# Kernel tuning notes

Measured on AMD Instinct MI355X. Metric: run time of the kernel, lower is better.

## Reference

```python
import jax, jax.numpy as jnp
import numpy as np

E, S, V_OBS, OBJ, H, L, V_COMM = 64, 64, 128, 16, 256, 32, 32
K = 2 * OBJ  # expected number of nonzero indices per step


def prelu(x, a):
    return jnp.where(x >= 0, x, a * x)


def setup_inputs() -> dict:
    key = jax.random.key(0)
    ks = jax.random.split(key, 32)
    # obs: multi-hot with exactly K ones per (episode, step)
    u = jax.random.uniform(ks[0], (E, S, V_OBS))
    idx = jnp.argsort(u, axis=-1)[..., :K]
    obs = jax.nn.one_hot(idx, V_OBS, dtype=jnp.float32).sum(-2)
    comm = jax.random.normal(ks[1], (E, S, L, V_COMM), jnp.float32)

    def w(k, shape):
        return (jax.random.normal(k, shape, jnp.float32) * 0.05)

    a = lambda: jnp.asarray(0.25, jnp.float32)  # PReLU init
    b = lambda n: jnp.full((n,), 0.01, jnp.float32)
    return dict(
        obs=obs, comm=comm,
        obs_emb=w(ks[2], (V_OBS, H)), obs_a_emb=a(),
        obs_W=w(ks[3], (K * H, H)), obs_b=b(H), obs_a=a(),
        comm_emb=w(ks[4], (V_COMM, H)), comm_a_emb=a(),
        cw1=w(ks[5], (H // 4, H, 1)), cb1=b(H // 4),
        cw3=w(ks[6], (H // 4, H, 3)), cb3=b(H // 4),
        cw5=w(ks[7], (H // 4, H, 5)), cb5=b(H // 4),
        cw7=w(ks[8], (H // 4, H, 7)), cb7=b(H // 4),
        bn_g=jnp.ones((H,), jnp.float32), bn_b=jnp.zeros((H,), jnp.float32), cnn_a=a(),
        Wx=w(ks[9], (3, H, H)), bx=jnp.full((3, H), 0.01, jnp.float32),
        Wh=w(ks[10], (3, H, H)), bh=jnp.full((3, H), 0.01, jnp.float32),
        lin_a1=a(), lin_W=w(ks[11], (H, H)), lin_b=b(H), lin_a2=a(),
    )


def reference(obs, comm, obs_emb, obs_a_emb, obs_W, obs_b, obs_a,
              comm_emb, comm_a_emb, cw1, cb1, cw3, cb3, cw5, cb5, cw7, cb7,
              bn_g, bn_b, cnn_a, Wx, bx, Wh, bh, lin_a1, lin_W, lin_b, lin_a2):
    Ep, St, _ = obs.shape
    # extract_and_concatenate: ascending indices of the K ones per (episode, step)
    idx = jnp.argsort(-obs, axis=-1)[..., :K]          # stable sort -> ascending nonzero idx
    oe = prelu(obs_emb[idx], obs_a_emb)                # [E,S,K,H]
    o = prelu(oe.reshape(Ep, St, K * H) @ obs_W + obs_b, obs_a)  # [E,S,H]

    # comm path (comm already at max_comm_len, pad_zeros is identity)
    tok = jnp.argmax(comm, axis=-1)                    # [E,S,L]
    ce = prelu(comm_emb[tok], comm_a_emb)              # [E,S,L,H]
    x = ce.reshape(Ep * St, L, H).transpose(0, 2, 1)   # [N,H,L]
    dn = ('NCH', 'OIH', 'NCH')
    conv = lambda w_, b_: jax.lax.conv_general_dilated(
        x, w_, (1,), 'SAME', dimension_numbers=dn) + b_[None, :, None]
    y = jnp.concatenate([conv(cw1, cb1), conv(cw3, cb3),
                         conv(cw5, cb5), conv(cw7, cb7)], axis=1)  # [N,H,L]
    # BatchNorm1d (training-mode batch statistics over N and L)
    m = y.mean(axis=(0, 2), keepdims=True)
    v = y.var(axis=(0, 2), keepdims=True)
    y = bn_g[None, :, None] * (y - m) / jnp.sqrt(v + 1e-5) + bn_b[None, :, None]
    y = prelu(y, cnn_a).transpose(0, 2, 1)             # [N,L,H]

    # MTRNN (time_constant=True -> new=1, old=0): GRU-like gated cell
    xproj = jnp.einsum('nlh,ghk->glnk', y, Wx) + bx[:, None, None, :]  # [3,L,N,H]
    h0 = jnp.zeros((Ep * St, H), y.dtype)

    def step(h, xs):
        xr, xz, xn = xs
        r = jax.nn.sigmoid(xr + h @ Wh[0] + bh[0])
        z = jax.nn.sigmoid(xz + h @ Wh[1] + bh[1])
        n = jnp.tanh(xn + r * (h @ Wh[2] + bh[2]))
        return n * (1 - z) + h * z, None

    hN, _ = jax.lax.scan(step, h0, (xproj[0], xproj[1], xproj[2]))  # last step == outputs[:,-1]
    c = hN.reshape(Ep, St, H)
    c = prelu(prelu(c, lin_a1) @ lin_W + lin_b, lin_a2)
    return jnp.concatenate([o, c], axis=-1)           # [E,S,2H]
```

## Files before the change

kernel.cpp:

```cpp
#include <hip/hip_runtime.h>
#include <hip/hip_bf16.h>

#define N_ 4096
#define VOBS 128
#define KOBS 32
#define H_ 256
#define L_ 32
#define VCOMM 32

typedef __attribute__((ext_vector_type(8))) short short8;
typedef __attribute__((ext_vector_type(4))) float floatx4;

__device__ __forceinline__ float prelu_f(float x, float a){ return x >= 0.f ? x : a*x; }
__device__ __forceinline__ ushort f2bf(float x){
  unsigned int u = __float_as_uint(x);
  u = (u + 0x7FFFu + ((u >> 16) & 1u)) >> 16;
  return (ushort)u;
}
__device__ __forceinline__ float bf2f(ushort x){
  unsigned int u = ((unsigned int)x) << 16;
  return __uint_as_float(u);
}

__device__ __forceinline__ void gl_lds16(const ushort* __restrict__ src, ushort* dst){
  __builtin_amdgcn_global_load_lds(
      (const __attribute__((address_space(1))) unsigned int*)src,
      (__attribute__((address_space(3))) unsigned int*)dst, 16, 0, 0);
}


__global__ __launch_bounds__(256) void k_idx(const float* __restrict__ obs, int* __restrict__ idx){
  const int n = blockIdx.x*4 + (threadIdx.x >> 6);
  const int lane = threadIdx.x & 63;
  float v0 = obs[(size_t)n*VOBS + lane];
  float v1 = obs[(size_t)n*VOBS + 64 + lane];
  unsigned long long m0 = __ballot(v0 > 0.5f);
  unsigned long long m1 = __ballot(v1 > 0.5f);
  unsigned long long lt = (1ull << lane) - 1ull;
  if (v0 > 0.5f){
    int pos = __popcll(m0 & lt);
    if (pos < KOBS) idx[n*KOBS + pos] = lane;
  }
  if (v1 > 0.5f){
    int pos = __popcll(m0) + __popcll(m1 & lt);
    if (pos < KOBS) idx[n*KOBS + pos] = 64 + lane;
  }
}

__global__ __launch_bounds__(256) void k_contrib(
    const float* __restrict__ obs_emb, const float* __restrict__ a_emb_p,
    const float* __restrict__ obs_W, float* __restrict__ contrib){
  const int k = blockIdx.x;
  const int vbase = blockIdx.y*16;
  const int tid = threadIdx.x;
  __shared__ float pe[16][H_];
  float a = a_emb_p[0];
  for (int i = tid; i < 16*H_; i += 256){
    int v = i >> 8, j = i & 255;
    pe[v][j] = prelu_f(obs_emb[(size_t)(vbase+v)*H_ + j], a);
  }
  __syncthreads();
  float acc[16];
  #pragma unroll
  for (int v = 0; v < 16; ++v) acc[v] = 0.f;
  for (int j = 0; j < H_; ++j){
    float w = obs_W[((size_t)(k*H_ + j))*H_ + tid];
    #pragma unroll
    for (int v = 0; v < 16; ++v) acc[v] += pe[v][j]*w;
  }
  for (int v = 0; v < 16; ++v)
    contrib[((size_t)((vbase+v)*KOBS + k))*H_ + tid] = acc[v];
}

__global__ __launch_bounds__(256) void k_obs_o(
    const int* __restrict__ idx, const float* __restrict__ contrib,
    const float* __restrict__ obs_b, const float* __restrict__ obs_a_p,
    float* __restrict__ out){
  const int n = blockIdx.x, tid = threadIdx.x;
  __shared__ int id[KOBS];
  if (tid < KOBS) id[tid] = idx[n*KOBS + tid];
  __syncthreads();
  float acc = obs_b[tid];
  #pragma unroll 8
  for (int k = 0; k < KOBS; ++k)
    acc += contrib[((size_t)(id[k]*KOBS + k))*H_ + tid];
  out[(size_t)n*512 + tid] = prelu_f(acc, obs_a_p[0]);
}


__global__ void k_tok(const float* __restrict__ comm, int* __restrict__ tok){
  int i = blockIdx.x*blockDim.x + threadIdx.x;
  if (i >= N_*L_) return;
  const float4* p = (const float4*)(comm + (size_t)i*VCOMM);
  float best = -1e30f; int bi = 0;
  #pragma unroll
  for (int j = 0; j < 8; ++j){
    float4 q = p[j];
    if (q.x > best){ best = q.x; bi = j*4+0; }
    if (q.y > best){ best = q.y; bi = j*4+1; }
    if (q.z > best){ best = q.z; bi = j*4+2; }
    if (q.w > best){ best = q.w; bi = j*4+3; }
  }
  tok[i] = bi;
}

__global__ void k_P(const float* __restrict__ comm_emb, const float* __restrict__ ca_p,
                    const float* __restrict__ cw1, const float* __restrict__ cw3,
                    const float* __restrict__ cw5, const float* __restrict__ cw7,
                    float* __restrict__ P){
  const int slot = blockIdx.x, v = blockIdx.y, c = threadIdx.x;
  int g, tap;
  if (slot == 0){ g=0; tap=0; }
  else if (slot < 4){ g=1; tap=slot-1; }
  else if (slot < 9){ g=2; tap=slot-4; }
  else { g=3; tap=slot-9; }
  const float* w; int ks;
  if (g==0){ w=cw1; ks=1; } else if (g==1){ w=cw3; ks=3; }
  else if (g==2){ w=cw5; ks=5; } else { w=cw7; ks=7; }
  float a = ca_p[0];
  float acc = 0.f;
  for (int h = 0; h < H_; ++h){
    float e = prelu_f(comm_emb[(size_t)v*H_ + h], a);
    acc += e * w[(size_t)(c*H_ + h)*ks + tap];
  }
  P[(size_t)(slot*VCOMM + v)*64 + c] = acc;
}

template<int KS, bool APPLY>
__device__ __forceinline__ void conv_work(
    const float* __restrict__ Ps, const int tk[16][L_], int wave, int lane,
    float bias, float scale, float shift, float ca,
    ushort* __restrict__ ynorm, int nbase, int g,
    float* s_out, float* q_out)
{
  constexpr int PAD = (KS-1)/2;
  float s = 0.f, sq = 0.f;
  for (int j = 0; j < 4; ++j){
    const int nn = wave*4 + j;
    int base[L_];
    #pragma unroll
    for (int l = 0; l < L_; ++l) base[l] = tk[nn][l]*64 + lane;
    #pragma unroll
    for (int l = 0; l < L_; ++l){
      float acc = bias;
      #pragma unroll
      for (int t = 0; t < KS; ++t){
        const int lp = l + t - PAD;
        if (lp >= 0 && lp < L_) acc += Ps[t*2048 + base[lp]];
      }
      if (APPLY){
        float y = prelu_f(fmaf(acc, scale, shift), ca);
        ynorm[((size_t)l*N_ + (nbase+nn))*H_ + g*64 + lane] = f2bf(y);
      } else {
        s += acc; sq += acc*acc;
      }
    }
  }
  *s_out = s; *q_out = sq;
}

__global__ __launch_bounds__(256) void k_conv_stats(
    const int* __restrict__ tok, const float* __restrict__ P,
    const float* __restrict__ cb1, const float* __restrict__ cb3,
    const float* __restrict__ cb5, const float* __restrict__ cb7,
    float* __restrict__ stats){
  const int g = blockIdx.y;
  const int nbase = blockIdx.x*16;
  const int tid = threadIdx.x, lane = tid & 63, wave = tid >> 6;
  const int ks = 2*g + 1, base = g*g;
  const float* cb = (g==0)?cb1:(g==1)?cb3:(g==2)?cb5:cb7;
  const float bias = cb[lane];
  __shared__ float Ps[7*2048];
  __shared__ int tk[16][L_];
  __shared__ float red_s[4][64], red_q[4][64];
  for (int i = tid; i < ks*512; i += 256)
    ((float4*)Ps)[i] = ((const float4*)(P + base*2048))[i];
  for (int i = tid; i < 16*L_; i += 256)
    tk[i>>5][i&31] = tok[(size_t)(nbase + (i>>5))*L_ + (i&31)];
  __syncthreads();
  float s = 0.f, sq = 0.f;
  switch (g){
    case 0: conv_work<1,false>(Ps, tk, wave, lane, bias, 0,0,0, nullptr, nbase, g, &s, &sq); break;
    case 1: conv_work<3,false>(Ps, tk, wave, lane, bias, 0,0,0, nullptr, nbase, g, &s, &sq); break;
    case 2: conv_work<5,false>(Ps, tk, wave, lane, bias, 0,0,0, nullptr, nbase, g, &s, &sq); break;
    default: conv_work<7,false>(Ps, tk, wave, lane, bias, 0,0,0, nullptr, nbase, g, &s, &sq); break;
  }
  red_s[wave][lane] = s; red_q[wave][lane] = sq;
  __syncthreads();
  if (wave == 0){
    float ts = red_s[0][lane]+red_s[1][lane]+red_s[2][lane]+red_s[3][lane];
    float tq = red_q[0][lane]+red_q[1][lane]+red_q[2][lane]+red_q[3][lane];
    atomicAdd(&stats[g*64 + lane], ts);
    atomicAdd(&stats[256 + g*64 + lane], tq);
  }
}

__global__ void k_bn_fin(const float* __restrict__ stats, const float* __restrict__ bn_g,
                         const float* __restrict__ bn_b, float* __restrict__ ss){
  int t = threadIdx.x;
  const float cnt = (float)(N_*L_);
  float m = stats[t]/cnt;
  float v = stats[256+t]/cnt - m*m;
  float sc = bn_g[t] / sqrtf(v + 1e-5f);
  ss[t] = sc; ss[256+t] = bn_b[t] - m*sc;
}

__global__ __launch_bounds__(256) void k_conv_apply(
    const int* __restrict__ tok, const float* __restrict__ P,
    const float* __restrict__ cb1, const float* __restrict__ cb3,
    const float* __restrict__ cb5, const float* __restrict__ cb7,
    const float* __restrict__ ss, const float* __restrict__ cnn_a_p,
    ushort* __restrict__ ynorm){
  const int g = blockIdx.y;
  const int nbase = blockIdx.x*16;
  const int tid = threadIdx.x, lane = tid & 63, wave = tid >> 6;
  const int ks = 2*g + 1, base = g*g;
  const float* cb = (g==0)?cb1:(g==1)?cb3:(g==2)?cb5:cb7;
  const float bias = cb[lane];
  const float scale = ss[g*64 + lane], shift = ss[256 + g*64 + lane];
  const float ca = cnn_a_p[0];
  __shared__ float Ps[7*2048];
  __shared__ int tk[16][L_];
  for (int i = tid; i < ks*512; i += 256)
    ((float4*)Ps)[i] = ((const float4*)(P + base*2048))[i];
  for (int i = tid; i < 16*L_; i += 256)
    tk[i>>5][i&31] = tok[(size_t)(nbase + (i>>5))*L_ + (i&31)];
  __syncthreads();
  float s, q;
  switch (g){
    case 0: conv_work<1,true>(Ps, tk, wave, lane, bias, scale, shift, ca, ynorm, nbase, g, &s, &q); break;
    case 1: conv_work<3,true>(Ps, tk, wave, lane, bias, scale, shift, ca, ynorm, nbase, g, &s, &q); break;
    case 2: conv_work<5,true>(Ps, tk, wave, lane, bias, scale, shift, ca, ynorm, nbase, g, &s, &q); break;
    default: conv_work<7,true>(Ps, tk, wave, lane, bias, scale, shift, ca, ynorm, nbase, g, &s, &q); break;
  }
}


__global__ void k_WT3(const float* __restrict__ Wx, const float* __restrict__ Wh,
                      ushort* __restrict__ WxT3, ushort* __restrict__ WhT3p){
  int id = blockIdx.x*256 + threadIdx.x;
  int g = id >> 16, u = (id >> 8) & 255, k = id & 255;
  WxT3[id]  = f2bf(Wx[(size_t)g*65536 + k*256 + u]);
  WhT3p[id] = f2bf(Wh[(size_t)g*65536 + k*256 + u]);
}

__global__ __launch_bounds__(256,2) void k_xproj(
    const ushort* __restrict__ Y, const ushort* __restrict__ WxT3,
    ushort* __restrict__ xp)
{
  extern __shared__ __align__(16) char smem[];
  ushort* Bs = (ushort*)smem;
  ushort* Tb = (ushort*)smem + 33792;
  const int bm = blockIdx.x;
  const int tid = threadIdx.x, lane = tid & 63, w = tid >> 6;
  const int wm = w >> 1, wn = w & 1;
  const int quad = lane >> 4, l16 = lane & 15;

  short8 Af[4][8];
  #pragma unroll
  for (int mi = 0; mi < 4; ++mi)
    #pragma unroll
    for (int kt = 0; kt < 8; ++kt)
      Af[mi][kt] = *(const short8*)(Y + ((size_t)(bm*128 + wm*64 + mi*16 + l16))*H_ + kt*32 + quad*8);

  for (int bn = 0; bn < 6; ++bn){
    __syncthreads();
    #pragma unroll
    for (int i = 0; i < 16; ++i){
      int id = i*256 + tid;
      int row = id >> 5, cc = id & 31;
      *(uint4*)&Bs[row*264 + cc*8] = *(const uint4*)(WxT3 + ((size_t)(bn*128 + row))*H_ + cc*8);
    }
    __syncthreads();
    floatx4 acc[4][4];
    #pragma unroll
    for (int i = 0; i < 4; ++i)
      #pragma unroll
      for (int j = 0; j < 4; ++j)
        acc[i][j] = (floatx4){0.f,0.f,0.f,0.f};
    #pragma unroll
    for (int kt = 0; kt < 8; ++kt){
      short8 b[4];
      #pragma unroll
      for (int ni = 0; ni < 4; ++ni)
        b[ni] = *(const short8*)&Bs[(wn*64 + ni*16 + l16)*264 + kt*32 + quad*8];
      #pragma unroll
      for (int mi = 0; mi < 4; ++mi)
        #pragma unroll
        for (int ni = 0; ni < 4; ++ni)
          acc[mi][ni] = __builtin_amdgcn_mfma_f32_16x16x32_bf16(Af[mi][kt], b[ni], acc[mi][ni], 0,0,0);
    }
    ushort* Tw = Tb + w*16*72;
    #pragma unroll
    for (int mi = 0; mi < 4; ++mi){
      #pragma unroll
      for (int ni = 0; ni < 4; ++ni)
        #pragma unroll
        for (int r = 0; r < 4; ++r)
          Tw[(quad*4 + r)*72 + ni*16 + l16] = f2bf(acc[mi][ni][r]);
      #pragma unroll
      for (int i = 0; i < 2; ++i){
        int rr = i*8 + (lane >> 3);
        int cc = lane & 7;
        int grow = bm*128 + wm*64 + mi*16 + rr;
        *(uint4*)(xp + (size_t)grow*768 + bn*128 + wn*64 + cc*8) = *(const uint4*)&Tw[rr*72 + cc*8];
      }
    }
  }
}

__global__ __launch_bounds__(512,2) void k_scan(
    const ushort* __restrict__ Whp, const ushort* __restrict__ xp,
    const float* __restrict__ bx, const float* __restrict__ bh,
    const float* __restrict__ h_in, const ushort* __restrict__ hbf_in,
    float* __restrict__ h_out, ushort* __restrict__ hbf_out, int first)
{
  extern __shared__ __align__(16) char smem[];
  ushort* hA = (ushort*)smem;
  float*  Ep = (float*)(smem + 8448);
  ushort* xs = (ushort*)(smem + 57856);

  const int tid = threadIdx.x;
  const int lane = tid & 63, w = tid >> 6;
  const int quad = lane >> 4, l16 = lane & 15;
  const int n0 = blockIdx.x*16;
  const int u = tid & 255, rq = tid >> 8;

  short8 Wf[6][8];
  #pragma unroll
  for (int ni = 0; ni < 6; ++ni)
    #pragma unroll
    for (int kt = 0; kt < 8; ++kt){
      Wf[ni][kt] = *(const short8*)(Whp + ((size_t)(w*96 + ni*16 + l16))*H_ + kt*32 + quad*8);
      asm volatile("" : "+v"(Wf[ni][kt]));
    }

  float hreg[8];
  if (first){
    #pragma unroll
    for (int r = 0; r < 8; ++r) hreg[r] = 0.f;
    for (int i = tid; i < 16*264; i += 512) hA[i] = 0;
  } else {
    #pragma unroll
    for (int r = 0; r < 8; ++r){
      int row = rq*8 + r;
      hreg[r] = h_in[(size_t)(n0+row)*H_ + u];
      hA[row*264 + u] = hbf_in[(size_t)(n0+row)*H_ + u];
    }
  }
  const float b0 = bx[u] + bh[u];
  const float b1 = bx[256+u] + bh[256+u];
  const float b2x = bx[512+u], b2h = bh[512+u];

  {
    const ushort* src = xp + (size_t)n0*768;
    #pragma unroll
    for (int t = 0; t < 3; ++t){
      int off = (w*3 + t)*512;
      gl_lds16(src + off + lane*8, xs + off);
    }
  }
  __syncthreads();

  for (int l = 0; l < 16; ++l){
    if (l < 15){
      const ushort* src = xp + (size_t)(l+1)*N_*768 + (size_t)n0*768;
      ushort* dst = xs + ((l+1)&1)*12288;
      #pragma unroll
      for (int t = 0; t < 3; ++t){
        int off = (w*3 + t)*512;
        gl_lds16(src + off + lane*8, dst + off);
      }
    }
    floatx4 acc[6];
    #pragma unroll
    for (int i = 0; i < 6; ++i) acc[i] = (floatx4){0.f,0.f,0.f,0.f};
    #pragma unroll
    for (int kt = 0; kt < 8; ++kt){
      short8 a = *(const short8*)&hA[l16*264 + kt*32 + quad*8];
      #pragma unroll
      for (int ni = 0; ni < 6; ++ni)
        acc[ni] = __builtin_amdgcn_mfma_f32_16x16x32_bf16(a, Wf[ni][kt], acc[ni], 0,0,0);
    }
    #pragma unroll
    for (int ni = 0; ni < 6; ++ni)
      #pragma unroll
      for (int r = 0; r < 4; ++r)
        Ep[(quad*4 + r)*772 + w*96 + ni*16 + l16] = acc[ni][r];
    __syncthreads();
    const ushort* xc = xs + (l&1)*12288;
    #pragma unroll
    for (int r = 0; r < 8; ++r){
      int row = rq*8 + r;
      float hr = Ep[row*772 +       u];
      float hz = Ep[row*772 + 256 + u];
      float hn = Ep[row*772 + 512 + u];
      float xr = bf2f(xc[row*768 +       u]);
      float xz = bf2f(xc[row*768 + 256 + u]);
      float xn = bf2f(xc[row*768 + 512 + u]);
      float rg = 1.f/(1.f + __expf(-(xr + hr + b0)));
      float zg = 1.f/(1.f + __expf(-(xz + hz + b1)));
      float na = xn + b2x + rg*(hn + b2h);
      float ng = 1.f - 2.f/(1.f + __expf(2.f*na));
      hreg[r] = ng*(1.f - zg) + hreg[r]*zg;
      hA[row*264 + u] = f2bf(hreg[r]);
    }
    __syncthreads();
  }
  #pragma unroll
  for (int r = 0; r < 8; ++r){
    int row = rq*8 + r;
    h_out[(size_t)(n0+row)*H_ + u] = hreg[r];
    hbf_out[(size_t)(n0+row)*H_ + u] = f2bf(hreg[r]);
  }
}

__global__ __launch_bounds__(256) void k_final(
    const float* __restrict__ h, const float* __restrict__ a1p,
    const float* __restrict__ lin_W, const float* __restrict__ lin_b,
    const float* __restrict__ a2p, float* __restrict__ out){
  const int nbase = blockIdx.x*16, tid = threadIdx.x;
  __shared__ float hp[16][H_];
  const float a1 = a1p[0], a2 = a2p[0];
  for (int i = tid; i < 16*H_; i += 256)
    hp[i>>8][i&255] = prelu_f(h[(size_t)(nbase + (i>>8))*H_ + (i&255)], a1);
  __syncthreads();
  float acc[16];
  const float b = lin_b[tid];
  #pragma unroll
  for (int r = 0; r < 16; ++r) acc[r] = b;
  for (int j = 0; j < H_; ++j){
    float w = lin_W[(size_t)j*H_ + tid];
    #pragma unroll
    for (int r = 0; r < 16; ++r) acc[r] += hp[r][j]*w;
  }
  for (int r = 0; r < 16; ++r)
    out[(size_t)(nbase+r)*512 + 256 + tid] = prelu_f(acc[r], a2);
}

extern "C" void kernel_launch(void* const* d_in, const int* in_sizes, int n_in,
                              void* d_out, int out_size, void* d_ws, size_t ws_size,
                              hipStream_t stream) {
  (void)in_sizes; (void)n_in; (void)out_size; (void)ws_size;
  const float* obs      = (const float*)d_in[0];
  const float* comm     = (const float*)d_in[1];
  const float* obs_emb  = (const float*)d_in[2];
  const float* obs_a_emb= (const float*)d_in[3];
  const float* obs_W    = (const float*)d_in[4];
  const float* obs_b    = (const float*)d_in[5];
  const float* obs_a    = (const float*)d_in[6];
  const float* comm_emb = (const float*)d_in[7];
  const float* comm_a   = (const float*)d_in[8];
  const float* cw1      = (const float*)d_in[9];
  const float* cb1      = (const float*)d_in[10];
  const float* cw3      = (const float*)d_in[11];
  const float* cb3      = (const float*)d_in[12];
  const float* cw5      = (const float*)d_in[13];
  const float* cb5      = (const float*)d_in[14];
  const float* cw7      = (const float*)d_in[15];
  const float* cb7      = (const float*)d_in[16];
  const float* bn_g     = (const float*)d_in[17];
  const float* bn_b     = (const float*)d_in[18];
  const float* cnn_a    = (const float*)d_in[19];
  const float* Wx       = (const float*)d_in[20];
  const float* bx       = (const float*)d_in[21];
  const float* Wh       = (const float*)d_in[22];
  const float* bh       = (const float*)d_in[23];
  const float* lin_a1   = (const float*)d_in[24];
  const float* lin_W    = (const float*)d_in[25];
  const float* lin_b    = (const float*)d_in[26];
  const float* lin_a2   = (const float*)d_in[27];
  float* out = (float*)d_out;

  char* ws = (char*)d_ws;
  float*  contrib = (float*)(ws + 0);
  float*  P       = (float*)(ws + 4194304);
  int*    idx     = (int*)  (ws + 4325376);
  int*    tok     = (int*)  (ws + 4849664);
  float*  stats   = (float*)(ws + 5373952);
  float*  ss      = (float*)(ws + 5376000);
  ushort* WxT3    = (ushort*)(ws + 5378048);
  ushort* WhT3p   = (ushort*)(ws + 5771264);
  float*  h_a     = (float*)(ws + 6164480);
  float*  h_b     = (float*)(ws + 10358784);
  ushort* hbf_a   = (ushort*)(ws + 14553088);
  ushort* hbf_b   = (ushort*)(ws + 16650240);
  ushort* ynorm   = (ushort*)(ws + 18747392);
  ushort* xp      = (ushort*)(ws + 85856256);

  hipMemsetAsync(stats, 0, 512*sizeof(float), stream);

  k_idx<<<1024, 256, 0, stream>>>(obs, idx);
  k_tok<<<512, 256, 0, stream>>>(comm, tok);
  k_WT3<<<768, 256, 0, stream>>>(Wx, Wh, WxT3, WhT3p);
  k_P<<<dim3(16,32), 64, 0, stream>>>(comm_emb, comm_a, cw1, cw3, cw5, cw7, P);
  k_contrib<<<dim3(32,8), 256, 0, stream>>>(obs_emb, obs_a_emb, obs_W, contrib);
  k_obs_o<<<4096, 256, 0, stream>>>(idx, contrib, obs_b, obs_a, out);
  k_conv_stats<<<dim3(256,4), 256, 0, stream>>>(tok, P, cb1, cb3, cb5, cb7, stats);
  k_bn_fin<<<1, 256, 0, stream>>>(stats, bn_g, bn_b, ss);
  k_conv_apply<<<dim3(256,4), 256, 0, stream>>>(tok, P, cb1, cb3, cb5, cb7, ss, cnn_a, ynorm);

  k_xproj<<<512, 256, 76800, stream>>>(ynorm, WxT3, xp);
  k_scan<<<256, 512, 107008, stream>>>(WhT3p, xp, bx, bh, h_a, hbf_a, h_a, hbf_a, 1);
  k_xproj<<<512, 256, 76800, stream>>>(ynorm + (size_t)16*N_*H_, WxT3, xp);
  k_scan<<<256, 512, 107008, stream>>>(WhT3p, xp, bx, bh, h_a, hbf_a, h_b, hbf_b, 0);

  k_final<<<256, 256, 0, stream>>>(h_b, lin_a1, lin_W, lin_b, lin_a2, out);
}
```

Before: 559.6 us.

## Compute GRU gates directly from MFMA accumulators in scan, dropping LDS staging

```diff
diff --git a/kernel.cpp b/kernel.cpp
--- a/kernel.cpp
+++ b/kernel.cpp
@@ -309,7 +309,7 @@
   }
 }
 
-__global__ __launch_bounds__(512,2) void k_scan(
+__global__ __launch_bounds__(512) void k_scan(
     const ushort* __restrict__ Whp, const ushort* __restrict__ xp,
     const float* __restrict__ bx, const float* __restrict__ bh,
     const float* __restrict__ h_in, const ushort* __restrict__ hbf_in,
@@ -317,40 +317,48 @@
 {
   extern __shared__ __align__(16) char smem[];
   ushort* hA = (ushort*)smem;
-  float*  Ep = (float*)(smem + 8448);
-  ushort* xs = (ushort*)(smem + 57856);
+  ushort* xs = (ushort*)(smem + 8448);
 
   const int tid = threadIdx.x;
   const int lane = tid & 63, w = tid >> 6;
   const int quad = lane >> 4, l16 = lane & 15;
   const int n0 = blockIdx.x*16;
-  const int u = tid & 255, rq = tid >> 8;
-
-  short8 Wf[6][8];
-  #pragma unroll
-  for (int ni = 0; ni < 6; ++ni)
+  const int u0 = w*32;
+
+  short8 Wf[2][8];
+  #pragma unroll
+  for (int t = 0; t < 2; ++t)
     #pragma unroll
     for (int kt = 0; kt < 8; ++kt){
-      Wf[ni][kt] = *(const short8*)(Whp + ((size_t)(w*96 + ni*16 + l16))*H_ + kt*32 + quad*8);
-      asm volatile("" : "+v"(Wf[ni][kt]));
-    }
-
-  float hreg[8];
+      Wf[t][kt] = *(const short8*)(Whp + ((size_t)(u0 + t*16 + l16))*H_ + kt*32 + quad*8);
+      asm volatile("" : "+v"(Wf[t][kt]));
+    }
+
+  float hreg[2][4];
   if (first){
     #pragma unroll
-    for (int r = 0; r < 8; ++r) hreg[r] = 0.f;
+    for (int t = 0; t < 2; ++t)
+      #pragma unroll
+      for (int r = 0; r < 4; ++r) hreg[t][r] = 0.f;
     for (int i = tid; i < 16*264; i += 512) hA[i] = 0;
   } else {
     #pragma unroll
-    for (int r = 0; r < 8; ++r){
-      int row = rq*8 + r;
-      hreg[r] = h_in[(size_t)(n0+row)*H_ + u];
-      hA[row*264 + u] = hbf_in[(size_t)(n0+row)*H_ + u];
-    }
-  }
-  const float b0 = bx[u] + bh[u];
-  const float b1 = bx[256+u] + bh[256+u];
-  const float b2x = bx[512+u], b2h = bh[512+u];
+    for (int t = 0; t < 2; ++t)
+      #pragma unroll
+      for (int r = 0; r < 4; ++r){
+        int row = quad*4 + r, u = u0 + t*16 + l16;
+        hreg[t][r] = h_in[(size_t)(n0+row)*H_ + u];
+        hA[row*264 + u] = hbf_in[(size_t)(n0+row)*H_ + u];
+      }
+  }
+  float c0[2], c1[2], c2x[2], c2h[2];
+  #pragma unroll
+  for (int t = 0; t < 2; ++t){
+    int u = u0 + t*16 + l16;
+    c0[t] = bx[u] + bh[u];
+    c1[t] = bx[256+u] + bh[256+u];
+    c2x[t] = bx[512+u]; c2h[t] = bh[512+u];
+  }
 
   {
     const ushort* src = xp + (size_t)n0*768;
@@ -372,47 +380,59 @@
         gl_lds16(src + off + lane*8, dst + off);
       }
     }
-    floatx4 acc[6];
-    #pragma unroll
-    for (int i = 0; i < 6; ++i) acc[i] = (floatx4){0.f,0.f,0.f,0.f};
+    floatx4 acc[3][2];
+    #pragma unroll
+    for (int g = 0; g < 3; ++g)
+      #pragma unroll
+      for (int t = 0; t < 2; ++t)
+        acc[g][t] = (floatx4){0.f,0.f,0.f,0.f};
     #pragma unroll
     for (int kt = 0; kt < 8; ++kt){
       short8 a = *(const short8*)&hA[l16*264 + kt*32 + quad*8];
-      #pragma unroll
-      for (int ni = 0; ni < 6; ++ni)
-        acc[ni] = __builtin_amdgcn_mfma_f32_16x16x32_bf16(a, Wf[ni][kt], acc[ni], 0,0,0);
-    }
-    #pragma unroll
-    for (int ni = 0; ni < 6; ++ni)
-      #pragma unroll
-      for (int r = 0; r < 4; ++r)
-        Ep[(quad*4 + r)*772 + w*96 + ni*16 + l16] = acc[ni][r];
+      short8 bs[2][2];
+      #pragma unroll
+      for (int g = 1; g < 3; ++g)
+        #pragma unroll
+        for (int t = 0; t < 2; ++t)
+          bs[g-1][t] = *(const short8*)(Whp + ((size_t)(g*256 + u0 + t*16 + l16))*H_ + kt*32 + quad*8);
+      #pragma unroll
+      for (int t = 0; t < 2; ++t)
+        acc[0][t] = __builtin_amdgcn_mfma_f32_16x16x32_bf16(a, Wf[t][kt], acc[0][t], 0,0,0);
+      #pragma unroll
+      for (int g = 1; g < 3; ++g)
+        #pragma unroll
+        for (int t = 0; t < 2; ++t)
+          acc[g][t] = __builtin_amdgcn_mfma_f32_16x16x32_bf16(a, bs[g-1][t], acc[g][t], 0,0,0);
+    }
     __syncthreads();
     const ushort* xc = xs + (l&1)*12288;
     #pragma unroll
-    for (int r = 0; r < 8; ++r){
-      int row = rq*8 + r;
-      float hr = Ep[row*772 +       u];
-      float hz = Ep[row*772 + 256 + u];
-      float hn = Ep[row*772 + 512 + u];
-      float xr = bf2f(xc[row*768 +       u]);
-      float xz = bf2f(xc[row*768 + 256 + u]);
-      float xn = bf2f(xc[row*768 + 512 + u]);
-      float rg = 1.f/(1.f + __expf(-(xr + hr + b0)));
-      float zg = 1.f/(1.f + __expf(-(xz + hz + b1)));
-      float na = xn + b2x + rg*(hn + b2h);
-      float ng = 1.f - 2.f/(1.f + __expf(2.f*na));
-      hreg[r] = ng*(1.f - zg) + hreg[r]*zg;
-      hA[row*264 + u] = f2bf(hreg[r]);
+    for (int t = 0; t < 2; ++t){
+      const int u = u0 + t*16 + l16;
+      #pragma unroll
+      for (int r = 0; r < 4; ++r){
+        const int row = quad*4 + r;
+        float xr = bf2f(xc[row*768 +       u]);
+        float xz = bf2f(xc[row*768 + 256 + u]);
+        float xn = bf2f(xc[row*768 + 512 + u]);
+        float rg = 1.f/(1.f + __expf(-(xr + acc[0][t][r] + c0[t])));
+        float zg = 1.f/(1.f + __expf(-(xz + acc[1][t][r] + c1[t])));
+        float na = xn + c2x[t] + rg*(acc[2][t][r] + c2h[t]);
+        float ng = 1.f - 2.f/(1.f + __expf(2.f*na));
+        hreg[t][r] = ng*(1.f - zg) + hreg[t][r]*zg;
+        hA[row*264 + u] = f2bf(hreg[t][r]);
+      }
     }
     __syncthreads();
   }
   #pragma unroll
-  for (int r = 0; r < 8; ++r){
-    int row = rq*8 + r;
-    h_out[(size_t)(n0+row)*H_ + u] = hreg[r];
-    hbf_out[(size_t)(n0+row)*H_ + u] = f2bf(hreg[r]);
-  }
+  for (int t = 0; t < 2; ++t)
+    #pragma unroll
+    for (int r = 0; r < 4; ++r){
+      int row = quad*4 + r, u = u0 + t*16 + l16;
+      h_out[(size_t)(n0+row)*H_ + u] = hreg[t][r];
+      hbf_out[(size_t)(n0+row)*H_ + u] = f2bf(hreg[t][r]);
+    }
 }
 
 __global__ __launch_bounds__(256) void k_final(
@@ -501,9 +521,9 @@
   k_conv_apply<<<dim3(256,4), 256, 0, stream>>>(tok, P, cb1, cb3, cb5, cb7, ss, cnn_a, ynorm);
 
   k_xproj<<<512, 256, 76800, stream>>>(ynorm, WxT3, xp);
-  k_scan<<<256, 512, 107008, stream>>>(WhT3p, xp, bx, bh, h_a, hbf_a, h_a, hbf_a, 1);
+  k_scan<<<256, 512, 57600, stream>>>(WhT3p, xp, bx, bh, h_a, hbf_a, h_a, hbf_a, 1);
   k_xproj<<<512, 256, 76800, stream>>>(ynorm + (size_t)16*N_*H_, WxT3, xp);
-  k_scan<<<256, 512, 107008, stream>>>(WhT3p, xp, bx, bh, h_a, hbf_a, h_b, hbf_b, 0);
+  k_scan<<<256, 512, 57600, stream>>>(WhT3p, xp, bx, bh, h_a, hbf_a, h_b, hbf_b, 0);
 
   k_final<<<256, 256, 0, stream>>>(h_b, lin_a1, lin_W, lin_b, lin_a2, out);
 }
```

New measurement: 578.4 us. +3.4%, slower.
